# Kernel tuning notes

Hardware: AMD Instinct MI355X
Metric: run time of the kernel (lower is better)

The kernel has to match this reference:

```python
import jax, jax.numpy as jnp
import numpy as np

B, N, D, H, LH, AH = 4, 2048, 512, 4, 64, 64
NUM_BUCKETS = 128
EPS = 1e-6
LENGTHS = np.array([2048, 1536, 1024, 1792])  # jagged per-sequence lengths, sum = 6400


def _ln(x, eps=EPS):
    # F.layer_norm without affine params (biased variance)
    m = jnp.mean(x, axis=-1, keepdims=True)
    v = jnp.var(x, axis=-1, keepdims=True)
    return (x - m) * jax.lax.rsqrt(v + eps)


def _rel_bias(all_timestamps, ts_w):
    # bucketed time-delta relative attention bias -> [B, N, N]
    delta = (all_timestamps[:, :, None] - all_timestamps[:, None, :]).astype(jnp.float32)
    bucket = jnp.clip(jnp.floor(jnp.log1p(jnp.abs(delta))).astype(jnp.int32), 0, NUM_BUCKETS)
    return ts_w[bucket]


def setup_inputs() -> dict:
    key = jax.random.key(0)
    ks = jax.random.split(key, 6)
    offsets = np.concatenate([[0], np.cumsum(LENGTHS)]).astype(np.int32)
    T = int(offsets[-1])
    token_batch = np.repeat(np.arange(B), LENGTHS).astype(np.int32)
    token_pos = np.concatenate([np.arange(l) for l in LENGTHS]).astype(np.int32)
    x = jax.random.normal(ks[0], (T, D), jnp.float32)
    uvqk = jax.random.normal(ks[1], (D, 2 * LH * H + 2 * AH * H), jnp.float32) * 0.02
    o_w = jax.random.normal(ks[2], (D, LH * H), jnp.float32) * 0.02  # torch Linear weight [out, in]
    o_b = jnp.zeros((D,), jnp.float32)
    ts_w = jax.random.normal(ks[3], (NUM_BUCKETS + 1,), jnp.float32) * 0.02
    all_timestamps = jnp.sort(jax.random.randint(ks[4], (B, N), 0, 1000000, jnp.int32), axis=-1)
    invalid_attn_mask = jnp.tril(jnp.ones((N, N), jnp.float32))  # causal validity mask in {0,1}
    return {
        'x': x, 'uvqk': uvqk, 'o_w': o_w, 'o_b': o_b, 'ts_w': ts_w,
        'all_timestamps': all_timestamps, 'invalid_attn_mask': invalid_attn_mask,
        'x_offsets': jnp.asarray(offsets), 'token_batch': jnp.asarray(token_batch),
        'token_pos': jnp.asarray(token_pos),
    }


def reference(x, uvqk, o_w, o_b, ts_w, all_timestamps, invalid_attn_mask,
              x_offsets, token_batch, token_pos):
    # input layernorm + fused uvqk projection with SiLU
    h = jax.nn.silu(_ln(x) @ uvqk)  # [T, 2*H*LH + 2*H*AH]
    u, v, q, k = jnp.split(h, [LH * H, 2 * LH * H, 2 * LH * H + AH * H], axis=1)

    def pad(vals):  # jagged [T, d] -> padded dense [B, N, d]
        return jnp.zeros((B, N, vals.shape[-1]), vals.dtype).at[token_batch, token_pos].set(vals)

    pq = pad(q).reshape(B, N, H, AH)
    pk = pad(k).reshape(B, N, H, AH)
    pv = pad(v).reshape(B, N, H, LH)

    scores = jnp.einsum('bnhd,bmhd->bhnm', pq, pk)
    scores = scores + _rel_bias(all_timestamps, ts_w)[:, None]  # broadcast over heads
    scores = jax.nn.silu(scores) / N
    scores = scores * invalid_attn_mask[None, None]
    attn = jnp.einsum('bhnm,bmhd->bnhd', scores, pv).reshape(B, N, H * LH)
    attn_j = attn[token_batch, token_pos]  # dense -> jagged [T, H*LH]

    o_in = u * _ln(attn_j)
    return o_in @ o_w.T + o_b + x
```

## Files before the change

kernel.cpp:

```cpp
#include <hip/hip_runtime.h>
#include <math.h>


typedef __attribute__((ext_vector_type(8))) short bf16x8;
typedef __attribute__((ext_vector_type(4))) float f32x4;

__device__ __forceinline__ float silu_f(float v) {
    return v / (1.0f + __expf(-v));
}

__device__ __forceinline__ unsigned short f2bf(float f) {
    unsigned int u = __float_as_uint(f);
    u += 0x7fffu + ((u >> 16) & 1u);
    return (unsigned short)(u >> 16);
}

__global__ __launch_bounds__(256) void k0_prep(const float* __restrict__ uvqk,
                                               unsigned short* __restrict__ uvqkT,
                                               const float* __restrict__ ow,
                                               unsigned short* __restrict__ owb) {
    const int tid = threadIdx.x;
    if (blockIdx.x < 128) {
        __shared__ float L[64][68];
        const int n0 = (blockIdx.x & 15) * 64;
        const int k0 = (blockIdx.x >> 4) * 64;
#pragma unroll
        for (int i = 0; i < 4; ++i) {
            const int r = (tid >> 4) + i * 16;
            const int c = (tid & 15) * 4;
            *(float4*)&L[r][c] = *(const float4*)(uvqk + (k0 + r) * 1024 + n0 + c);
        }
        __syncthreads();
        const int n = tid >> 2;
        const int kb = (tid & 3) * 16;
#pragma unroll
        for (int pass = 0; pass < 2; ++pass) {
            unsigned short pk[8];
#pragma unroll
            for (int j = 0; j < 8; ++j) pk[j] = f2bf(L[kb + pass * 8 + j][n]);
            *(uint4*)(uvqkT + (n0 + n) * 512 + k0 + kb + pass * 8) = *(const uint4*)pk;
        }
    } else {
        const int base = ((blockIdx.x - 128) * 256 + tid) * 8;
        float4 a = *(const float4*)(ow + base);
        float4 b = *(const float4*)(ow + base + 4);
        unsigned short pk[8] = {f2bf(a.x), f2bf(a.y), f2bf(a.z), f2bf(a.w),
                                f2bf(b.x), f2bf(b.y), f2bf(b.z), f2bf(b.w)};
        *(uint4*)(owb + base) = *(const uint4*)pk;
    }
}

__global__ __launch_bounds__(256) void k1_ln(const float* __restrict__ x,
                                             unsigned short* __restrict__ xnb) {
    const int row = blockIdx.x;
    const int tid = threadIdx.x;
    const float* xr = x + row * 512;
    float a = xr[tid];
    float b = xr[tid + 256];
    float s = a + b, ss = a * a + b * b;
#pragma unroll
    for (int off = 32; off > 0; off >>= 1) {
        s += __shfl_down(s, off);
        ss += __shfl_down(ss, off);
    }
    __shared__ float red[8];
    if ((tid & 63) == 0) { red[tid >> 6] = s; red[4 + (tid >> 6)] = ss; }
    __syncthreads();
    s = red[0] + red[1] + red[2] + red[3];
    ss = red[4] + red[5] + red[6] + red[7];
    const float mean = s * (1.0f / 512.0f);
    const float var = ss * (1.0f / 512.0f) - mean * mean;
    const float rstd = rsqrtf(var + 1e-6f);
    xnb[row * 512 + tid] = f2bf((a - mean) * rstd);
    xnb[row * 512 + tid + 256] = f2bf((b - mean) * rstd);
}

__global__ __launch_bounds__(256, 4) void k2_gemm1(const unsigned short* __restrict__ A,
                                                   const unsigned short* __restrict__ Bt,
                                                   float* __restrict__ u_out,
                                                   unsigned short* __restrict__ hb) {
    __shared__ __align__(16) unsigned short As[64][72];
    __shared__ __align__(16) unsigned short Bs[64][72];
    const int tid = threadIdx.x;
    const int lane = tid & 63;
    const int w = tid >> 6;
    const int l15 = lane & 15;
    const int quad = lane >> 4;
    const int bm = blockIdx.y * 64;
    const int bn = blockIdx.x * 64;

    f32x4 acc[4] = {};
    for (int kc = 0; kc < 512; kc += 64) {
        __syncthreads();
#pragma unroll
        for (int i = 0; i < 2; ++i) {
            const int r = (tid >> 3) + i * 32;
            const int c = (tid & 7) * 8;
            *(uint4*)&As[r][c] = *(const uint4*)(A + (bm + r) * 512 + kc + c);
            *(uint4*)&Bs[r][c] = *(const uint4*)(Bt + (bn + r) * 512 + kc + c);
        }
        __syncthreads();
        const bf16x8 a0 = *(const bf16x8*)&As[w * 16 + l15][quad * 8];
        const bf16x8 a1 = *(const bf16x8*)&As[w * 16 + l15][32 + quad * 8];
#pragma unroll
        for (int nt = 0; nt < 4; ++nt) {
            bf16x8 b0 = *(const bf16x8*)&Bs[nt * 16 + l15][quad * 8];
            bf16x8 b1 = *(const bf16x8*)&Bs[nt * 16 + l15][32 + quad * 8];
            acc[nt] = __builtin_amdgcn_mfma_f32_16x16x32_bf16(a0, b0, acc[nt], 0, 0, 0);
            acc[nt] = __builtin_amdgcn_mfma_f32_16x16x32_bf16(a1, b1, acc[nt], 0, 0, 0);
        }
    }
    const int m = bm + w * 16 + quad * 4;
    if (bn < 256) {
#pragma unroll
        for (int nt = 0; nt < 4; ++nt)
#pragma unroll
            for (int reg = 0; reg < 4; ++reg)
                u_out[(m + reg) * 256 + bn + nt * 16 + l15] = silu_f(acc[nt][reg]);
    } else {
#pragma unroll
        for (int nt = 0; nt < 4; ++nt)
#pragma unroll
            for (int reg = 0; reg < 4; ++reg)
                hb[(m + reg) * 768 + (bn - 256) + nt * 16 + l15] = f2bf(silu_f(acc[nt][reg]));
    }
}

__global__ __launch_bounds__(256) void k0c_transpose_v(const unsigned short* __restrict__ hb,
                                                       unsigned short* __restrict__ vtb) {
    __shared__ unsigned short L[64][72];
    const int tb = blockIdx.x;
    const int db = blockIdx.y;
    const int tid = threadIdx.x;
#pragma unroll
    for (int i = 0; i < 2; ++i) {
        const int r = (tid >> 3) + i * 32, c = (tid & 7) * 8;
        *(uint4*)&L[r][c] = *(const uint4*)(hb + (tb * 64 + r) * 768 + db * 64 + c);
    }
    __syncthreads();
#pragma unroll
    for (int i = 0; i < 2; ++i) {
        const int r = (tid >> 3) + i * 32, c = (tid & 7) * 8;
        unsigned short pk[8];
#pragma unroll
        for (int j = 0; j < 8; ++j) pk[j] = L[c + j][r];
        *(uint4*)(vtb + (db * 64 + r) * 6400 + tb * 64 + c) = *(const uint4*)pk;
    }
}

__global__ __launch_bounds__(256, 5) void k3_attn(const unsigned short* __restrict__ hb,
                                                  const unsigned short* __restrict__ vtb,
                                                  const int* __restrict__ ts,
                                                  const float* __restrict__ tsw,
                                                  const int* __restrict__ offs,
                                                  float* __restrict__ part) {
    const int qt = 31 - (blockIdx.x & 31);
    const int c = blockIdx.x >> 5;
    const int b = blockIdx.y;
    const int hd = blockIdx.z;
    const int off = offs[b];
    const int len = offs[b + 1] - off;
    const int nqt = len >> 6;
    if (qt >= nqt || c * 4 > qt) return;
    const int q0 = qt * 64;
    const int kt_lo = c * 4;
    const int kt_hi = min(qt, c * 4 + 3);

    __shared__ __align__(16) unsigned short QPs[64][72];
    __shared__ __align__(16) unsigned short Ks[64][72];
    __shared__ __align__(16) unsigned short Vt[64][72];
    __shared__ float tqf[64], tkf[64];
    __shared__ float tw[132];

    const int tid = threadIdx.x;
    const int lane = tid & 63;
    const int w = tid >> 6;
    const int l15 = lane & 15;
    const int quad = lane >> 4;
    const int sr = tid >> 3;
    const int sc = (tid & 7) * 8;

    if (tid < 129) tw[tid] = tsw[tid];
    if (tid < 64) tqf[tid] = (float)ts[b * 2048 + q0 + tid];
#pragma unroll
    for (int i = 0; i < 2; ++i)
        *(uint4*)&QPs[sr + i * 32][sc] =
            *(const uint4*)(hb + (off + q0 + sr + i * 32) * 768 + 256 + hd * 64 + sc);
    __syncthreads();

    const bf16x8 aQ0 = *(const bf16x8*)&QPs[w * 16 + l15][quad * 8];
    const bf16x8 aQ1 = *(const bf16x8*)&QPs[w * 16 + l15][32 + quad * 8];
    const f32x4 tq4 = *(const f32x4*)&tqf[w * 16 + quad * 4];
    const int nbase = q0 + w * 16 + quad * 4;

    f32x4 oacc[4] = {};

    for (int kt = kt_lo; kt <= kt_hi; ++kt) {
        const int m0 = kt * 64;
        __syncthreads();
#pragma unroll
        for (int i = 0; i < 2; ++i) {
            const int r = sr + i * 32;
            *(uint4*)&Ks[r][sc] =
                *(const uint4*)(hb + (off + m0 + r) * 768 + 512 + hd * 64 + sc);
            *(uint4*)&Vt[r][sc] =
                *(const uint4*)(vtb + (hd * 64 + r) * 6400 + off + m0 + sc);
        }
        if (tid < 64) tkf[tid] = (float)ts[b * 2048 + m0 + tid];
        __syncthreads();

        f32x4 s[4] = {};
#pragma unroll
        for (int nt = 0; nt < 4; ++nt) {
            bf16x8 b0 = *(const bf16x8*)&Ks[nt * 16 + l15][quad * 8];
            bf16x8 b1 = *(const bf16x8*)&Ks[nt * 16 + l15][32 + quad * 8];
            s[nt] = __builtin_amdgcn_mfma_f32_16x16x32_bf16(aQ0, b0, s[nt], 0, 0, 0);
            s[nt] = __builtin_amdgcn_mfma_f32_16x16x32_bf16(aQ1, b1, s[nt], 0, 0, 0);
        }

        const bool diag = (kt == qt);
#pragma unroll
        for (int nt = 0; nt < 4; ++nt) {
            const int m = m0 + nt * 16 + l15;
            const float tk = tkf[nt * 16 + l15];
#pragma unroll
            for (int reg = 0; reg < 4; ++reg) {
                const float delta = fabsf(tq4[reg] - tk);
                int bucket = (int)floorf(__log2f(1.0f + delta) * 0.6931471805599453f);
                bucket = bucket < 0 ? 0 : (bucket > 128 ? 128 : bucket);
                float val = s[nt][reg] + tw[bucket];
                val = silu_f(val) * (1.0f / 2048.0f);
                if (diag) val = (m <= nbase + reg) ? val : 0.0f;
                QPs[w * 16 + quad * 4 + reg][nt * 16 + l15] = f2bf(val);
            }
        }

        const bf16x8 aP0 = *(const bf16x8*)&QPs[w * 16 + l15][quad * 8];
        const bf16x8 aP1 = *(const bf16x8*)&QPs[w * 16 + l15][32 + quad * 8];
#pragma unroll
        for (int nt = 0; nt < 4; ++nt) {
            bf16x8 v0 = *(const bf16x8*)&Vt[nt * 16 + l15][quad * 8];
            bf16x8 v1 = *(const bf16x8*)&Vt[nt * 16 + l15][32 + quad * 8];
            oacc[nt] = __builtin_amdgcn_mfma_f32_16x16x32_bf16(aP0, v0, oacc[nt], 0, 0, 0);
            oacc[nt] = __builtin_amdgcn_mfma_f32_16x16x32_bf16(aP1, v1, oacc[nt], 0, 0, 0);
        }
    }

    float* pc = part + (size_t)c * (6400 * 256);
#pragma unroll
    for (int nt = 0; nt < 4; ++nt)
#pragma unroll
        for (int reg = 0; reg < 4; ++reg)
            pc[(off + q0 + w * 16 + quad * 4 + reg) * 256 + hd * 64 + nt * 16 + l15] =
                oacc[nt][reg];
}

__global__ __launch_bounds__(256) void k4a_ln(const float* __restrict__ part,
                                              const float* __restrict__ u_in,
                                              const int* __restrict__ token_pos,
                                              unsigned short* __restrict__ o_in) {
    const int row = blockIdx.x;
    const int tid = threadIdx.x;
    const int qt = token_pos[row] >> 6;
    const int nch = (qt + 4) >> 2;
    float a = 0.0f;
    for (int c = 0; c < nch; ++c) a += part[(size_t)c * (6400 * 256) + row * 256 + tid];
    float s = a, ss = a * a;
#pragma unroll
    for (int off = 32; off > 0; off >>= 1) {
        s += __shfl_down(s, off);
        ss += __shfl_down(ss, off);
    }
    __shared__ float red[8];
    if ((tid & 63) == 0) { red[tid >> 6] = s; red[4 + (tid >> 6)] = ss; }
    __syncthreads();
    s = red[0] + red[1] + red[2] + red[3];
    ss = red[4] + red[5] + red[6] + red[7];
    const float mean = s * (1.0f / 256.0f);
    const float var = ss * (1.0f / 256.0f) - mean * mean;
    const float rstd = rsqrtf(var + 1e-6f);
    const float u = u_in[row * 256 + tid];
    o_in[row * 256 + tid] = f2bf(u * (a - mean) * rstd);
}

__global__ __launch_bounds__(256, 4) void k4b_gemm2(const unsigned short* __restrict__ A,
                                                    const unsigned short* __restrict__ owb,
                                                    const float* __restrict__ ob,
                                                    const float* __restrict__ x,
                                                    float* __restrict__ out) {
    __shared__ __align__(16) unsigned short As[64][72];
    __shared__ __align__(16) unsigned short Bs[64][72];
    const int tid = threadIdx.x;
    const int lane = tid & 63;
    const int w = tid >> 6;
    const int l15 = lane & 15;
    const int quad = lane >> 4;
    const int bm = blockIdx.y * 64;
    const int bn = blockIdx.x * 64;

    f32x4 acc[4] = {};
    for (int kc = 0; kc < 256; kc += 64) {
        __syncthreads();
#pragma unroll
        for (int i = 0; i < 2; ++i) {
            const int r = (tid >> 3) + i * 32;
            const int c = (tid & 7) * 8;
            *(uint4*)&As[r][c] = *(const uint4*)(A + (bm + r) * 256 + kc + c);
            *(uint4*)&Bs[r][c] = *(const uint4*)(owb + (bn + r) * 256 + kc + c);
        }
        __syncthreads();
        const bf16x8 a0 = *(const bf16x8*)&As[w * 16 + l15][quad * 8];
        const bf16x8 a1 = *(const bf16x8*)&As[w * 16 + l15][32 + quad * 8];
#pragma unroll
        for (int nt = 0; nt < 4; ++nt) {
            bf16x8 b0 = *(const bf16x8*)&Bs[nt * 16 + l15][quad * 8];
            bf16x8 b1 = *(const bf16x8*)&Bs[nt * 16 + l15][32 + quad * 8];
            acc[nt] = __builtin_amdgcn_mfma_f32_16x16x32_bf16(a0, b0, acc[nt], 0, 0, 0);
            acc[nt] = __builtin_amdgcn_mfma_f32_16x16x32_bf16(a1, b1, acc[nt], 0, 0, 0);
        }
    }
    const int m = bm + w * 16 + quad * 4;
#pragma unroll
    for (int nt = 0; nt < 4; ++nt) {
        const int d = bn + nt * 16 + l15;
        const float bias = ob[d];
#pragma unroll
        for (int reg = 0; reg < 4; ++reg)
            out[(m + reg) * 512 + d] = acc[nt][reg] + bias + x[(m + reg) * 512 + d];
    }
}

extern "C" void kernel_launch(void* const* d_in, const int* in_sizes, int n_in,
                              void* d_out, int out_size, void* d_ws, size_t ws_size,
                              hipStream_t stream) {
    const float* x = (const float*)d_in[0];
    const float* uvqk = (const float*)d_in[1];
    const float* ow = (const float*)d_in[2];
    const float* ob = (const float*)d_in[3];
    const float* tsw = (const float*)d_in[4];
    const int* ts = (const int*)d_in[5];
    const int* offs = (const int*)d_in[7];
    const int* token_pos = (const int*)d_in[9];
    float* out = (float*)d_out;

    float* ws = (float*)d_ws;
    float* u = ws;
    float* part = u + 6400 * 256;
    unsigned short* xnb = (unsigned short*)(part + 8 * 6400 * 256);
    unsigned short* hb = xnb + 6400 * 512;
    unsigned short* o_in = hb + 6400 * 768;
    unsigned short* uvqkT = o_in + 6400 * 256;
    unsigned short* owb = uvqkT + 1024 * 512;
    unsigned short* vtb = xnb;

    k0_prep<<<192, 256, 0, stream>>>(uvqk, uvqkT, ow, owb);
    k1_ln<<<6400, 256, 0, stream>>>(x, xnb);
    k2_gemm1<<<dim3(16, 100), 256, 0, stream>>>(xnb, uvqkT, u, hb);
    k0c_transpose_v<<<dim3(100, 4), 256, 0, stream>>>(hb, vtb);
    k3_attn<<<dim3(256, 4, 4), 256, 0, stream>>>(hb, vtb, ts, tsw, offs, part);
    k4a_ln<<<6400, 256, 0, stream>>>(part, u, token_pos, o_in);
    k4b_gemm2<<<dim3(8, 100), 256, 0, stream>>>(o_in, owb, ob, x, out);
}
```

Baseline: 178.1 us.

## Fuse weight prep into layernorm, write transposed V from GEMM epilogue

Merges the weight-conversion kernel into the input layernorm kernel as extra blocks, and has the projection GEMM write V already transposed through shared memory, which removes the separate transpose kernel and two launches. V^T now gets its own workspace region instead of reusing xnb. In the attention inner loop the bucket clamp and floor are dropped, and SiLU/N uses a hardware reciprocal. Dropping the clamp relies on bucket indices staying in range for non-negative deltas, and rcp slightly lowers precision.

```diff
diff --git a/kernel.cpp b/kernel.cpp
--- a/kernel.cpp
+++ b/kernel.cpp
@@ -5,8 +5,12 @@
 typedef __attribute__((ext_vector_type(8))) short bf16x8;
 typedef __attribute__((ext_vector_type(4))) float f32x4;
 
+__device__ __forceinline__ float silu_over_2048(float v) {
+    return v * __builtin_amdgcn_rcpf(2048.0f + 2048.0f * __expf(-v));
+}
+
 __device__ __forceinline__ float silu_f(float v) {
-    return v / (1.0f + __expf(-v));
+    return v * __builtin_amdgcn_rcpf(1.0f + __expf(-v));
 }
 
 __device__ __forceinline__ unsigned short f2bf(float f) {
@@ -15,15 +19,39 @@
     return (unsigned short)(u >> 16);
 }
 
-__global__ __launch_bounds__(256) void k0_prep(const float* __restrict__ uvqk,
-                                               unsigned short* __restrict__ uvqkT,
-                                               const float* __restrict__ ow,
-                                               unsigned short* __restrict__ owb) {
-    const int tid = threadIdx.x;
-    if (blockIdx.x < 128) {
-        __shared__ float L[64][68];
-        const int n0 = (blockIdx.x & 15) * 64;
-        const int k0 = (blockIdx.x >> 4) * 64;
+__global__ __launch_bounds__(256) void k1_ln_prep(const float* __restrict__ x,
+                                                  unsigned short* __restrict__ xnb,
+                                                  const float* __restrict__ uvqk,
+                                                  unsigned short* __restrict__ uvqkT,
+                                                  const float* __restrict__ ow,
+                                                  unsigned short* __restrict__ owb) {
+    __shared__ float L[64][68];
+    const int tid = threadIdx.x;
+    const int bx = blockIdx.x;
+    if (bx < 6400) {
+        const float* xr = x + bx * 512;
+        float a = xr[tid];
+        float b = xr[tid + 256];
+        float s = a + b, ss = a * a + b * b;
+#pragma unroll
+        for (int off = 32; off > 0; off >>= 1) {
+            s += __shfl_down(s, off);
+            ss += __shfl_down(ss, off);
+        }
+        float* red = &L[0][0];
+        if ((tid & 63) == 0) { red[tid >> 6] = s; red[4 + (tid >> 6)] = ss; }
+        __syncthreads();
+        s = red[0] + red[1] + red[2] + red[3];
+        ss = red[4] + red[5] + red[6] + red[7];
+        const float mean = s * (1.0f / 512.0f);
+        const float var = ss * (1.0f / 512.0f) - mean * mean;
+        const float rstd = rsqrtf(var + 1e-6f);
+        xnb[bx * 512 + tid] = f2bf((a - mean) * rstd);
+        xnb[bx * 512 + tid + 256] = f2bf((b - mean) * rstd);
+    } else if (bx < 6528) {
+        const int t = bx - 6400;
+        const int n0 = (t & 15) * 64;
+        const int k0 = (t >> 4) * 64;
 #pragma unroll
         for (int i = 0; i < 4; ++i) {
             const int r = (tid >> 4) + i * 16;
@@ -41,7 +69,7 @@
             *(uint4*)(uvqkT + (n0 + n) * 512 + k0 + kb + pass * 8) = *(const uint4*)pk;
         }
     } else {
-        const int base = ((blockIdx.x - 128) * 256 + tid) * 8;
+        const int base = ((bx - 6528) * 256 + tid) * 8;
         float4 a = *(const float4*)(ow + base);
         float4 b = *(const float4*)(ow + base + 4);
         unsigned short pk[8] = {f2bf(a.x), f2bf(a.y), f2bf(a.z), f2bf(a.w),
@@ -50,35 +78,11 @@
     }
 }
 
-__global__ __launch_bounds__(256) void k1_ln(const float* __restrict__ x,
-                                             unsigned short* __restrict__ xnb) {
-    const int row = blockIdx.x;
-    const int tid = threadIdx.x;
-    const float* xr = x + row * 512;
-    float a = xr[tid];
-    float b = xr[tid + 256];
-    float s = a + b, ss = a * a + b * b;
-#pragma unroll
-    for (int off = 32; off > 0; off >>= 1) {
-        s += __shfl_down(s, off);
-        ss += __shfl_down(ss, off);
-    }
-    __shared__ float red[8];
-    if ((tid & 63) == 0) { red[tid >> 6] = s; red[4 + (tid >> 6)] = ss; }
-    __syncthreads();
-    s = red[0] + red[1] + red[2] + red[3];
-    ss = red[4] + red[5] + red[6] + red[7];
-    const float mean = s * (1.0f / 512.0f);
-    const float var = ss * (1.0f / 512.0f) - mean * mean;
-    const float rstd = rsqrtf(var + 1e-6f);
-    xnb[row * 512 + tid] = f2bf((a - mean) * rstd);
-    xnb[row * 512 + tid + 256] = f2bf((b - mean) * rstd);
-}
-
 __global__ __launch_bounds__(256, 4) void k2_gemm1(const unsigned short* __restrict__ A,
                                                    const unsigned short* __restrict__ Bt,
                                                    float* __restrict__ u_out,
-                                                   unsigned short* __restrict__ hb) {
+                                                   unsigned short* __restrict__ hb,
+                                                   unsigned short* __restrict__ vtb) {
     __shared__ __align__(16) unsigned short As[64][72];
     __shared__ __align__(16) unsigned short Bs[64][72];
     const int tid = threadIdx.x;
@@ -117,34 +121,29 @@
 #pragma unroll
             for (int reg = 0; reg < 4; ++reg)
                 u_out[(m + reg) * 256 + bn + nt * 16 + l15] = silu_f(acc[nt][reg]);
+    } else if (bn < 512) {
+        __syncthreads();
+#pragma unroll
+        for (int nt = 0; nt < 4; ++nt) {
+            unsigned short pk[4];
+#pragma unroll
+            for (int reg = 0; reg < 4; ++reg) pk[reg] = f2bf(silu_f(acc[nt][reg]));
+            *(uint2*)&As[nt * 16 + l15][w * 16 + quad * 4] = *(const uint2*)pk;
+        }
+        __syncthreads();
+        const int sr = tid >> 3, sc = (tid & 7) * 8;
+#pragma unroll
+        for (int i = 0; i < 2; ++i) {
+            const int r = sr + i * 32;
+            *(uint4*)(vtb + (size_t)(bn - 256 + r) * 6400 + bm + sc) =
+                *(const uint4*)&As[r][sc];
+        }
     } else {
 #pragma unroll
         for (int nt = 0; nt < 4; ++nt)
 #pragma unroll
             for (int reg = 0; reg < 4; ++reg)
                 hb[(m + reg) * 768 + (bn - 256) + nt * 16 + l15] = f2bf(silu_f(acc[nt][reg]));
-    }
-}
-
-__global__ __launch_bounds__(256) void k0c_transpose_v(const unsigned short* __restrict__ hb,
-                                                       unsigned short* __restrict__ vtb) {
-    __shared__ unsigned short L[64][72];
-    const int tb = blockIdx.x;
-    const int db = blockIdx.y;
-    const int tid = threadIdx.x;
-#pragma unroll
-    for (int i = 0; i < 2; ++i) {
-        const int r = (tid >> 3) + i * 32, c = (tid & 7) * 8;
-        *(uint4*)&L[r][c] = *(const uint4*)(hb + (tb * 64 + r) * 768 + db * 64 + c);
-    }
-    __syncthreads();
-#pragma unroll
-    for (int i = 0; i < 2; ++i) {
-        const int r = (tid >> 3) + i * 32, c = (tid & 7) * 8;
-        unsigned short pk[8];
-#pragma unroll
-        for (int j = 0; j < 8; ++j) pk[j] = L[c + j][r];
-        *(uint4*)(vtb + (db * 64 + r) * 6400 + tb * 64 + c) = *(const uint4*)pk;
     }
 }
 
@@ -204,7 +203,7 @@
             *(uint4*)&Ks[r][sc] =
                 *(const uint4*)(hb + (off + m0 + r) * 768 + 512 + hd * 64 + sc);
             *(uint4*)&Vt[r][sc] =
-                *(const uint4*)(vtb + (hd * 64 + r) * 6400 + off + m0 + sc);
+                *(const uint4*)(vtb + (size_t)(hd * 64 + r) * 6400 + off + m0 + sc);
         }
         if (tid < 64) tkf[tid] = (float)ts[b * 2048 + m0 + tid];
         __syncthreads();
@@ -226,12 +225,11 @@
 #pragma unroll
             for (int reg = 0; reg < 4; ++reg) {
                 const float delta = fabsf(tq4[reg] - tk);
-                int bucket = (int)floorf(__log2f(1.0f + delta) * 0.6931471805599453f);
-                bucket = bucket < 0 ? 0 : (bucket > 128 ? 128 : bucket);
+                const int bucket = (int)(__log2f(1.0f + delta) * 0.6931471805599453f);
                 float val = s[nt][reg] + tw[bucket];
-                val = silu_f(val) * (1.0f / 2048.0f);
-                if (diag) val = (m <= nbase + reg) ? val : 0.0f;
-                QPs[w * 16 + quad * 4 + reg][nt * 16 + l15] = f2bf(val);
+                float p = silu_over_2048(val);
+                if (diag) p = (m <= nbase + reg) ? p : 0.0f;
+                QPs[w * 16 + quad * 4 + reg][nt * 16 + l15] = f2bf(p);
             }
         }
 
@@ -351,12 +349,10 @@
     unsigned short* o_in = hb + 6400 * 768;
     unsigned short* uvqkT = o_in + 6400 * 256;
     unsigned short* owb = uvqkT + 1024 * 512;
-    unsigned short* vtb = xnb;
-
-    k0_prep<<<192, 256, 0, stream>>>(uvqk, uvqkT, ow, owb);
-    k1_ln<<<6400, 256, 0, stream>>>(x, xnb);
-    k2_gemm1<<<dim3(16, 100), 256, 0, stream>>>(xnb, uvqkT, u, hb);
-    k0c_transpose_v<<<dim3(100, 4), 256, 0, stream>>>(hb, vtb);
+    unsigned short* vtb = owb + 512 * 256;
+
+    k1_ln_prep<<<6592, 256, 0, stream>>>(x, xnb, uvqk, uvqkT, ow, owb);
+    k2_gemm1<<<dim3(16, 100), 256, 0, stream>>>(xnb, uvqkT, u, hb, vtb);
     k3_attn<<<dim3(256, 4, 4), 256, 0, stream>>>(hb, vtb, ts, tsw, offs, part);
     k4a_ln<<<6400, 256, 0, stream>>>(part, u, token_pos, o_in);
     k4b_gemm2<<<dim3(8, 100), 256, 0, stream>>>(o_in, owb, ob, x, out);
```

Result: faster. 162.7 us (-8.6%).
